# Kernel optimization log

Hardware: AMD Instinct MI355X
Metric: run time of the kernel (lower is better)

Reference implementation:

```python
import jax, jax.numpy as jnp
import numpy as np

TOP_K = 0.7  # fraction of highest-loss samples kept


def setup_inputs() -> dict:
    key = jax.random.key(0)
    k1, k2 = jax.random.split(key)
    N, C = 262144, 128
    inp = jax.random.normal(k1, (N, C), dtype=jnp.float32)
    tgt = jax.random.randint(k2, (N,), 0, C, dtype=jnp.int64)
    return {"input": inp, "target": tgt}


def reference(input, target):
    # log-softmax over classes, one stable pass
    logp = jax.nn.log_softmax(input, axis=-1)  # [N, C]
    # per-row NLL: -logp[i, target[i]]
    per_row = -jnp.take_along_axis(logp, target[:, None], axis=-1)[:, 0]  # [N]
    k = int(TOP_K * per_row.shape[0])
    top_vals, _ = jax.lax.top_k(per_row, k)  # k largest losses
    return jnp.mean(top_vals)
```

## Files before the change

### kernel.cpp

```cpp
#include <hip/hip_runtime.h>


#define NCLASS 128
#define NREP 8

struct Scalars {
  unsigned sel1, sel2;
  unsigned cnt_above;
  int krem;
  unsigned thr_bits;
  unsigned pad[11];
};

__device__ __forceinline__ unsigned suffix_incl_u(unsigned x, int lane) {
#pragma unroll
  for (int off = 1; off < 64; off <<= 1) {
    unsigned v = __shfl_down(x, off, 64);
    if (lane + off < 64) x += v;
  }
  return x;
}

__global__ __launch_bounds__(256) void loss_hist_kernel(
    const float* __restrict__ x, const int* __restrict__ tgt,
    float* __restrict__ losses, unsigned* __restrict__ hist1, int N) {
  __shared__ unsigned lh[4096];
  for (int i = threadIdx.x; i < 4096; i += 256) lh[i] = 0;
  __syncthreads();

  const int lane = threadIdx.x & 63;
  const int j = lane & 7;
  const int r = lane >> 3;
  const int gw = blockIdx.x * 4 + (threadIdx.x >> 6);
  const int W = gridDim.x * 4;

  for (int base = gw; base * 8 < N; base += W) {
    const int row = base * 8 + r;
    const float4* rp = (const float4*)(x + (size_t)row * NCLASS);
    float4 a = rp[j];
    float4 b = rp[j + 8];
    float4 c = rp[j + 16];
    float4 d = rp[j + 24];
    int t = tgt[row];
    float xt = x[(size_t)row * NCLASS + t];

    float m = fmaxf(fmaxf(fmaxf(a.x, a.y), fmaxf(a.z, a.w)),
                    fmaxf(fmaxf(b.x, b.y), fmaxf(b.z, b.w)));
    m = fmaxf(m, fmaxf(fmaxf(c.x, c.y), fmaxf(c.z, c.w)));
    m = fmaxf(m, fmaxf(fmaxf(d.x, d.y), fmaxf(d.z, d.w)));
    m = fmaxf(m, __shfl_xor(m, 1, 64));
    m = fmaxf(m, __shfl_xor(m, 2, 64));
    m = fmaxf(m, __shfl_xor(m, 4, 64));

    float s = __expf(a.x - m) + __expf(a.y - m) + __expf(a.z - m) + __expf(a.w - m)
            + __expf(b.x - m) + __expf(b.y - m) + __expf(b.z - m) + __expf(b.w - m)
            + __expf(c.x - m) + __expf(c.y - m) + __expf(c.z - m) + __expf(c.w - m)
            + __expf(d.x - m) + __expf(d.y - m) + __expf(d.z - m) + __expf(d.w - m);
    s += __shfl_xor(s, 1, 64);
    s += __shfl_xor(s, 2, 64);
    s += __shfl_xor(s, 4, 64);

    if (j == 0) {
      float loss = fmaxf(__logf(s) + m - xt, 0.0f);
      losses[row] = loss;
      atomicAdd(&lh[__float_as_uint(loss) >> 20], 1u);
    }
  }
  __syncthreads();
  unsigned* h = hist1 + (size_t)(blockIdx.x & (NREP - 1)) * 4096;
  for (int i = threadIdx.x; i < 4096; i += 256) {
    unsigned v = lh[i];
    if (v) atomicAdd(&h[i], v);
  }
}

__global__ __launch_bounds__(256) void hist_refine_kernel(
    const float* __restrict__ losses, const Scalars* __restrict__ sc,
    unsigned* __restrict__ hist, int N, int phase) {
  __shared__ unsigned lh[1024];
  for (int i = threadIdx.x; i < 1024; i += 256) lh[i] = 0;
  __syncthreads();
  unsigned prefix, shift;
  if (phase == 1) { prefix = sc->sel1; shift = 20; }
  else { prefix = (sc->sel1 << 10) | sc->sel2; shift = 10; }
  const unsigned sub_shift = shift - 10;
  const float4* L4 = (const float4*)losses;
  const int n4 = N >> 2;
  for (int idx = blockIdx.x * 256 + threadIdx.x; idx < n4; idx += gridDim.x * 256) {
    float4 v = L4[idx];
    unsigned b;
    b = __float_as_uint(v.x); if ((b >> shift) == prefix) atomicAdd(&lh[(b >> sub_shift) & 1023u], 1u);
    b = __float_as_uint(v.y); if ((b >> shift) == prefix) atomicAdd(&lh[(b >> sub_shift) & 1023u], 1u);
    b = __float_as_uint(v.z); if ((b >> shift) == prefix) atomicAdd(&lh[(b >> sub_shift) & 1023u], 1u);
    b = __float_as_uint(v.w); if ((b >> shift) == prefix) atomicAdd(&lh[(b >> sub_shift) & 1023u], 1u);
  }
  __syncthreads();
  unsigned* h = hist + (size_t)(blockIdx.x & (NREP - 1)) * 1024;
  for (int i = threadIdx.x; i < 1024; i += 256) {
    unsigned v = lh[i];
    if (v) atomicAdd(&h[i], v);
  }
}

__global__ void scan_kernel(const unsigned* __restrict__ hist, Scalars* sc,
                            int nbins, int phase, int K) {
  const int lane = threadIdx.x;
  const int bpt = nbins >> 6;
  const int Ktar = (phase == 0) ? K : sc->krem;

  unsigned csum = 0;
  for (int rr = 0; rr < NREP; ++rr) {
    const uint4* h4 = (const uint4*)(hist + (size_t)rr * nbins + lane * bpt);
    for (int i = 0; i < (bpt >> 2); ++i) {
      uint4 q = h4[i];
      csum += q.x + q.y + q.z + q.w;
    }
  }
  unsigned suf = suffix_incl_u(csum, lane);
  unsigned long long mask = __ballot(suf >= (unsigned)Ktar);
  int c = 63 - __builtin_clzll(mask);
  unsigned above_excl = suf - csum;
  unsigned aboveC = __shfl(above_excl, c, 64);

  unsigned h = 0;
  if (lane < bpt)
    for (int rr = 0; rr < NREP; ++rr) h += hist[(size_t)rr * nbins + c * bpt + lane];
  unsigned suf2 = suffix_incl_u(h, lane);
  unsigned long long mask2 = __ballot((lane < bpt) && (aboveC + suf2 >= (unsigned)Ktar));
  int u = 63 - __builtin_clzll(mask2);
  unsigned hU = __shfl(h, u, 64);
  unsigned suf2U = __shfl(suf2, u, 64);
  unsigned above = aboveC + suf2U - hU;
  int bin = c * bpt + u;

  if (lane == 0) {
    if (phase == 0) {
      sc->sel1 = (unsigned)bin; sc->cnt_above = above; sc->krem = Ktar - (int)above;
    } else if (phase == 1) {
      sc->sel2 = (unsigned)bin; sc->cnt_above += above; sc->krem = Ktar - (int)above;
    } else {
      sc->thr_bits = (sc->sel1 << 20) | (sc->sel2 << 10) | (unsigned)bin;
      sc->cnt_above += above;
    }
  }
}

__global__ __launch_bounds__(256) void sum_topk_kernel(
    const float* __restrict__ losses, const Scalars* __restrict__ sc,
    double* __restrict__ partials, int N) {
  const unsigned thr = sc->thr_bits;
  double acc = 0.0;
  const float4* L4 = (const float4*)losses;
  const int n4 = N >> 2;
  for (int idx = blockIdx.x * 256 + threadIdx.x; idx < n4; idx += gridDim.x * 256) {
    float4 v = L4[idx];
    if (__float_as_uint(v.x) > thr) acc += v.x;
    if (__float_as_uint(v.y) > thr) acc += v.y;
    if (__float_as_uint(v.z) > thr) acc += v.z;
    if (__float_as_uint(v.w) > thr) acc += v.w;
  }
#pragma unroll
  for (int off = 32; off > 0; off >>= 1) acc += __shfl_down(acc, off, 64);
  __shared__ double wsum[4];
  if ((threadIdx.x & 63) == 0) wsum[threadIdx.x >> 6] = acc;
  __syncthreads();
  if (threadIdx.x == 0)
    partials[blockIdx.x] = wsum[0] + wsum[1] + wsum[2] + wsum[3];
}

__global__ void finalize_kernel(const double* __restrict__ partials,
                                const Scalars* __restrict__ sc,
                                float* __restrict__ out, int K, int npart) {
  const int lane = threadIdx.x;
  double s = 0.0;
  for (int i = lane; i < npart; i += 64) s += partials[i];
#pragma unroll
  for (int off = 32; off > 0; off >>= 1) s += __shfl_down(s, off, 64);
  if (lane == 0) {
    double thr = (double)__uint_as_float(sc->thr_bits);
    double mean = (s + (double)(K - (int)sc->cnt_above) * thr) / (double)K;
    *out = (float)mean;
  }
}

extern "C" void kernel_launch(void* const* d_in, const int* in_sizes, int n_in,
                              void* d_out, int out_size, void* d_ws, size_t ws_size,
                              hipStream_t stream) {
  const float* x = (const float*)d_in[0];
  const int* tgt = (const int*)d_in[1];
  float* out = (float*)d_out;
  const int N = in_sizes[1];
  const int K = (int)(0.7 * (double)N);

  char* ws = (char*)d_ws;
  const size_t OFF_H1 = (size_t)N * 4;
  const size_t OFF_H2 = OFF_H1 + (size_t)NREP * 4096 * 4;
  const size_t OFF_H3 = OFF_H2 + (size_t)NREP * 1024 * 4;
  const size_t OFF_SC = OFF_H3 + (size_t)NREP * 1024 * 4;
  const size_t OFF_PT = OFF_SC + 256;

  float* losses = (float*)ws;
  unsigned* hist1 = (unsigned*)(ws + OFF_H1);
  unsigned* hist2 = (unsigned*)(ws + OFF_H2);
  unsigned* hist3 = (unsigned*)(ws + OFF_H3);
  Scalars* sc = (Scalars*)(ws + OFF_SC);
  double* partials = (double*)(ws + OFF_PT);

  hipMemsetAsync(ws + OFF_H1, 0, OFF_PT - OFF_H1, stream);

  loss_hist_kernel<<<512, 256, 0, stream>>>(x, tgt, losses, hist1, N);
  scan_kernel<<<1, 64, 0, stream>>>(hist1, sc, 4096, 0, K);
  hist_refine_kernel<<<64, 256, 0, stream>>>(losses, sc, hist2, N, 1);
  scan_kernel<<<1, 64, 0, stream>>>(hist2, sc, 1024, 1, K);
  hist_refine_kernel<<<64, 256, 0, stream>>>(losses, sc, hist3, N, 2);
  scan_kernel<<<1, 64, 0, stream>>>(hist3, sc, 1024, 2, K);
  sum_topk_kernel<<<128, 256, 0, stream>>>(losses, sc, partials, N);
  finalize_kernel<<<1, 64, 0, stream>>>(partials, sc, out, K, 128);
}
```

Measured before the change: 228.2 us.

## Fuse all phases into one cooperative persistent kernel with grid syncs

Replaces the memset plus eight separate kernel launches with one cooperative mega-kernel that runs loss computation, three radix-histogram refinement passes, scans, the top-k sum and finalisation, separated by grid-wide syncs. The grid is sized from occupancy queries so every CU is filled, and histogram zeroing moves inside the kernel. This removes per-launch overhead and the small single-block scan launches between phases. In exchange it adds eight grid barriers and host-side attribute and occupancy queries on every call, and falls back to the old launch path if cooperative launch is unavailable.

```diff
diff --git a/kernel.cpp b/kernel.cpp
--- a/kernel.cpp
+++ b/kernel.cpp
@@ -1,15 +1,19 @@
 #include <hip/hip_runtime.h>
+#include <hip/hip_cooperative_groups.h>
+
+namespace cg = cooperative_groups;
 
 
 #define NCLASS 128
 #define NREP 8
+#define TPB 256
+#define MAXGRID 2048
 
 struct Scalars {
   unsigned sel1, sel2;
   unsigned cnt_above;
   int krem;
   unsigned thr_bits;
-  unsigned pad[11];
 };
 
 __device__ __forceinline__ unsigned suffix_incl_u(unsigned x, int lane) {
@@ -21,89 +25,8 @@
   return x;
 }
 
-__global__ __launch_bounds__(256) void loss_hist_kernel(
-    const float* __restrict__ x, const int* __restrict__ tgt,
-    float* __restrict__ losses, unsigned* __restrict__ hist1, int N) {
-  __shared__ unsigned lh[4096];
-  for (int i = threadIdx.x; i < 4096; i += 256) lh[i] = 0;
-  __syncthreads();
-
-  const int lane = threadIdx.x & 63;
-  const int j = lane & 7;
-  const int r = lane >> 3;
-  const int gw = blockIdx.x * 4 + (threadIdx.x >> 6);
-  const int W = gridDim.x * 4;
-
-  for (int base = gw; base * 8 < N; base += W) {
-    const int row = base * 8 + r;
-    const float4* rp = (const float4*)(x + (size_t)row * NCLASS);
-    float4 a = rp[j];
-    float4 b = rp[j + 8];
-    float4 c = rp[j + 16];
-    float4 d = rp[j + 24];
-    int t = tgt[row];
-    float xt = x[(size_t)row * NCLASS + t];
-
-    float m = fmaxf(fmaxf(fmaxf(a.x, a.y), fmaxf(a.z, a.w)),
-                    fmaxf(fmaxf(b.x, b.y), fmaxf(b.z, b.w)));
-    m = fmaxf(m, fmaxf(fmaxf(c.x, c.y), fmaxf(c.z, c.w)));
-    m = fmaxf(m, fmaxf(fmaxf(d.x, d.y), fmaxf(d.z, d.w)));
-    m = fmaxf(m, __shfl_xor(m, 1, 64));
-    m = fmaxf(m, __shfl_xor(m, 2, 64));
-    m = fmaxf(m, __shfl_xor(m, 4, 64));
-
-    float s = __expf(a.x - m) + __expf(a.y - m) + __expf(a.z - m) + __expf(a.w - m)
-            + __expf(b.x - m) + __expf(b.y - m) + __expf(b.z - m) + __expf(b.w - m)
-            + __expf(c.x - m) + __expf(c.y - m) + __expf(c.z - m) + __expf(c.w - m)
-            + __expf(d.x - m) + __expf(d.y - m) + __expf(d.z - m) + __expf(d.w - m);
-    s += __shfl_xor(s, 1, 64);
-    s += __shfl_xor(s, 2, 64);
-    s += __shfl_xor(s, 4, 64);
-
-    if (j == 0) {
-      float loss = fmaxf(__logf(s) + m - xt, 0.0f);
-      losses[row] = loss;
-      atomicAdd(&lh[__float_as_uint(loss) >> 20], 1u);
-    }
-  }
-  __syncthreads();
-  unsigned* h = hist1 + (size_t)(blockIdx.x & (NREP - 1)) * 4096;
-  for (int i = threadIdx.x; i < 4096; i += 256) {
-    unsigned v = lh[i];
-    if (v) atomicAdd(&h[i], v);
-  }
-}
-
-__global__ __launch_bounds__(256) void hist_refine_kernel(
-    const float* __restrict__ losses, const Scalars* __restrict__ sc,
-    unsigned* __restrict__ hist, int N, int phase) {
-  __shared__ unsigned lh[1024];
-  for (int i = threadIdx.x; i < 1024; i += 256) lh[i] = 0;
-  __syncthreads();
-  unsigned prefix, shift;
-  if (phase == 1) { prefix = sc->sel1; shift = 20; }
-  else { prefix = (sc->sel1 << 10) | sc->sel2; shift = 10; }
-  const unsigned sub_shift = shift - 10;
-  const float4* L4 = (const float4*)losses;
-  const int n4 = N >> 2;
-  for (int idx = blockIdx.x * 256 + threadIdx.x; idx < n4; idx += gridDim.x * 256) {
-    float4 v = L4[idx];
-    unsigned b;
-    b = __float_as_uint(v.x); if ((b >> shift) == prefix) atomicAdd(&lh[(b >> sub_shift) & 1023u], 1u);
-    b = __float_as_uint(v.y); if ((b >> shift) == prefix) atomicAdd(&lh[(b >> sub_shift) & 1023u], 1u);
-    b = __float_as_uint(v.z); if ((b >> shift) == prefix) atomicAdd(&lh[(b >> sub_shift) & 1023u], 1u);
-    b = __float_as_uint(v.w); if ((b >> shift) == prefix) atomicAdd(&lh[(b >> sub_shift) & 1023u], 1u);
-  }
-  __syncthreads();
-  unsigned* h = hist + (size_t)(blockIdx.x & (NREP - 1)) * 1024;
-  for (int i = threadIdx.x; i < 1024; i += 256) {
-    unsigned v = lh[i];
-    if (v) atomicAdd(&h[i], v);
-  }
-}
-
-__global__ void scan_kernel(const unsigned* __restrict__ hist, Scalars* sc,
-                            int nbins, int phase, int K) {
+__device__ void scan_phase(const unsigned* __restrict__ hist, Scalars* sc,
+                           int nbins, int phase, int K) {
   const int lane = threadIdx.x;
   const int bpt = nbins >> 6;
   const int Ktar = (phase == 0) ? K : sc->krem;
@@ -145,14 +68,235 @@
   }
 }
 
-__global__ __launch_bounds__(256) void sum_topk_kernel(
+__device__ __forceinline__ void loss_hist_body(
+    const float* __restrict__ x, const int* __restrict__ tgt,
+    float* __restrict__ losses, unsigned* __restrict__ hist1,
+    unsigned* lh, int N, int nblocks) {
+  const int lane = threadIdx.x & 63;
+  const int j = lane & 7;
+  const int r = lane >> 3;
+  const int gw = blockIdx.x * (TPB / 64) + (threadIdx.x >> 6);
+  const int W = nblocks * (TPB / 64);
+  for (int base = gw; base * 8 < N; base += W) {
+    const int row = base * 8 + r;
+    const float4* rp = (const float4*)(x + (size_t)row * NCLASS);
+    float4 a = rp[j];
+    float4 b = rp[j + 8];
+    float4 c = rp[j + 16];
+    float4 d = rp[j + 24];
+    int t = tgt[row];
+    float xt = x[(size_t)row * NCLASS + t];
+
+    float m = fmaxf(fmaxf(fmaxf(a.x, a.y), fmaxf(a.z, a.w)),
+                    fmaxf(fmaxf(b.x, b.y), fmaxf(b.z, b.w)));
+    m = fmaxf(m, fmaxf(fmaxf(c.x, c.y), fmaxf(c.z, c.w)));
+    m = fmaxf(m, fmaxf(fmaxf(d.x, d.y), fmaxf(d.z, d.w)));
+    m = fmaxf(m, __shfl_xor(m, 1, 64));
+    m = fmaxf(m, __shfl_xor(m, 2, 64));
+    m = fmaxf(m, __shfl_xor(m, 4, 64));
+
+    float s = __expf(a.x - m) + __expf(a.y - m) + __expf(a.z - m) + __expf(a.w - m)
+            + __expf(b.x - m) + __expf(b.y - m) + __expf(b.z - m) + __expf(b.w - m)
+            + __expf(c.x - m) + __expf(c.y - m) + __expf(c.z - m) + __expf(c.w - m)
+            + __expf(d.x - m) + __expf(d.y - m) + __expf(d.z - m) + __expf(d.w - m);
+    s += __shfl_xor(s, 1, 64);
+    s += __shfl_xor(s, 2, 64);
+    s += __shfl_xor(s, 4, 64);
+
+    if (j == 0) {
+      float loss = fmaxf(__logf(s) + m - xt, 0.0f);
+      losses[row] = loss;
+      atomicAdd(&lh[__float_as_uint(loss) >> 20], 1u);
+    }
+  }
+  __syncthreads();
+  unsigned* h = hist1 + (size_t)(blockIdx.x & (NREP - 1)) * 4096;
+  for (int i = threadIdx.x; i < 4096; i += TPB) {
+    unsigned v = lh[i];
+    if (v) atomicAdd(&h[i], v);
+  }
+}
+
+__global__ __launch_bounds__(TPB, 2) void mega_kernel(
+    const float* __restrict__ x, const int* __restrict__ tgt,
+    float* __restrict__ losses, unsigned* __restrict__ hist1,
+    unsigned* __restrict__ hist2, unsigned* __restrict__ hist3,
+    Scalars* __restrict__ sc, double* __restrict__ partials,
+    float* __restrict__ out, int N, int K) {
+  cg::grid_group grid = cg::this_grid();
+  __shared__ unsigned lh[4096];
+  __shared__ double dsm[TPB / 64];
+
+  const int lane = threadIdx.x & 63;
+  const int G = gridDim.x;
+
+  for (int i = threadIdx.x; i < 4096; i += TPB) lh[i] = 0;
+  for (int i = blockIdx.x * TPB + threadIdx.x; i < NREP * 4096; i += G * TPB)
+    hist1[i] = 0;
+  __syncthreads();
+  grid.sync();
+
+  loss_hist_body(x, tgt, losses, hist1, lh, N, G);
+  __threadfence();
+  grid.sync();
+
+  if (blockIdx.x == 0) {
+    if (threadIdx.x < 64) scan_phase(hist1, sc, 4096, 0, K);
+  } else {
+    for (int i = (blockIdx.x - 1) * TPB + threadIdx.x; i < NREP * 1024;
+         i += (G - 1) * TPB)
+      hist2[i] = 0;
+  }
+  __threadfence();
+  grid.sync();
+
+  const float4* L4 = (const float4*)losses;
+  const int n4 = N >> 2;
+
+  {
+    for (int i = threadIdx.x; i < 1024; i += TPB) lh[i] = 0;
+    __syncthreads();
+    const unsigned prefix = sc->sel1;
+    for (int idx = blockIdx.x * TPB + threadIdx.x; idx < n4; idx += G * TPB) {
+      float4 v = L4[idx];
+      unsigned b;
+      b = __float_as_uint(v.x); if ((b >> 20) == prefix) atomicAdd(&lh[(b >> 10) & 1023u], 1u);
+      b = __float_as_uint(v.y); if ((b >> 20) == prefix) atomicAdd(&lh[(b >> 10) & 1023u], 1u);
+      b = __float_as_uint(v.z); if ((b >> 20) == prefix) atomicAdd(&lh[(b >> 10) & 1023u], 1u);
+      b = __float_as_uint(v.w); if ((b >> 20) == prefix) atomicAdd(&lh[(b >> 10) & 1023u], 1u);
+    }
+    __syncthreads();
+    unsigned* h = hist2 + (size_t)(blockIdx.x & (NREP - 1)) * 1024;
+    for (int i = threadIdx.x; i < 1024; i += TPB) {
+      unsigned v = lh[i];
+      if (v) atomicAdd(&h[i], v);
+    }
+  }
+  __threadfence();
+  grid.sync();
+
+  if (blockIdx.x == 0) {
+    if (threadIdx.x < 64) scan_phase(hist2, sc, 1024, 1, K);
+  } else {
+    for (int i = (blockIdx.x - 1) * TPB + threadIdx.x; i < NREP * 1024;
+         i += (G - 1) * TPB)
+      hist3[i] = 0;
+  }
+  __threadfence();
+  grid.sync();
+
+  {
+    for (int i = threadIdx.x; i < 1024; i += TPB) lh[i] = 0;
+    __syncthreads();
+    const unsigned prefix = (sc->sel1 << 10) | sc->sel2;
+    for (int idx = blockIdx.x * TPB + threadIdx.x; idx < n4; idx += G * TPB) {
+      float4 v = L4[idx];
+      unsigned b;
+      b = __float_as_uint(v.x); if ((b >> 10) == prefix) atomicAdd(&lh[b & 1023u], 1u);
+      b = __float_as_uint(v.y); if ((b >> 10) == prefix) atomicAdd(&lh[b & 1023u], 1u);
+      b = __float_as_uint(v.z); if ((b >> 10) == prefix) atomicAdd(&lh[b & 1023u], 1u);
+      b = __float_as_uint(v.w); if ((b >> 10) == prefix) atomicAdd(&lh[b & 1023u], 1u);
+    }
+    __syncthreads();
+    unsigned* h = hist3 + (size_t)(blockIdx.x & (NREP - 1)) * 1024;
+    for (int i = threadIdx.x; i < 1024; i += TPB) {
+      unsigned v = lh[i];
+      if (v) atomicAdd(&h[i], v);
+    }
+  }
+  __threadfence();
+  grid.sync();
+
+  if (blockIdx.x == 0 && threadIdx.x < 64) scan_phase(hist3, sc, 1024, 2, K);
+  __threadfence();
+  grid.sync();
+
+  {
+    const unsigned thr = sc->thr_bits;
+    double acc = 0.0;
+    for (int idx = blockIdx.x * TPB + threadIdx.x; idx < n4; idx += G * TPB) {
+      float4 v = L4[idx];
+      if (__float_as_uint(v.x) > thr) acc += v.x;
+      if (__float_as_uint(v.y) > thr) acc += v.y;
+      if (__float_as_uint(v.z) > thr) acc += v.z;
+      if (__float_as_uint(v.w) > thr) acc += v.w;
+    }
+#pragma unroll
+    for (int off = 32; off > 0; off >>= 1) acc += __shfl_down(acc, off, 64);
+    if (lane == 0) dsm[threadIdx.x >> 6] = acc;
+    __syncthreads();
+    if (threadIdx.x == 0)
+      partials[blockIdx.x] = dsm[0] + dsm[1] + dsm[2] + dsm[3];
+  }
+  __threadfence();
+  grid.sync();
+
+  if (blockIdx.x == 0) {
+    double s = 0.0;
+    for (int i = threadIdx.x; i < G; i += TPB) s += partials[i];
+#pragma unroll
+    for (int off = 32; off > 0; off >>= 1) s += __shfl_down(s, off, 64);
+    if (lane == 0) dsm[threadIdx.x >> 6] = s;
+    __syncthreads();
+    if (threadIdx.x == 0) {
+      double thrv = (double)__uint_as_float(sc->thr_bits);
+      double mean = (dsm[0] + dsm[1] + dsm[2] + dsm[3] +
+                     (double)(K - (int)sc->cnt_above) * thrv) / (double)K;
+      *out = (float)mean;
+    }
+  }
+}
+
+__global__ __launch_bounds__(TPB) void loss_hist_kernel(
+    const float* __restrict__ x, const int* __restrict__ tgt,
+    float* __restrict__ losses, unsigned* __restrict__ hist1, int N, int nblocks) {
+  __shared__ unsigned lh[4096];
+  for (int i = threadIdx.x; i < 4096; i += TPB) lh[i] = 0;
+  __syncthreads();
+  loss_hist_body(x, tgt, losses, hist1, lh, N, nblocks);
+}
+
+__global__ void scan_kernel(const unsigned* __restrict__ hist, Scalars* sc,
+                            int nbins, int phase, int K) {
+  scan_phase(hist, sc, nbins, phase, K);
+}
+
+__global__ __launch_bounds__(TPB) void hist_refine_kernel(
+    const float* __restrict__ losses, const Scalars* __restrict__ sc,
+    unsigned* __restrict__ hist, int N, int phase) {
+  __shared__ unsigned lh[1024];
+  for (int i = threadIdx.x; i < 1024; i += TPB) lh[i] = 0;
+  __syncthreads();
+  unsigned prefix, shift;
+  if (phase == 1) { prefix = sc->sel1; shift = 20; }
+  else { prefix = (sc->sel1 << 10) | sc->sel2; shift = 10; }
+  const unsigned sub_shift = shift - 10;
+  const float4* L4 = (const float4*)losses;
+  const int n4 = N >> 2;
+  for (int idx = blockIdx.x * TPB + threadIdx.x; idx < n4; idx += gridDim.x * TPB) {
+    float4 v = L4[idx];
+    unsigned b;
+    b = __float_as_uint(v.x); if ((b >> shift) == prefix) atomicAdd(&lh[(b >> sub_shift) & 1023u], 1u);
+    b = __float_as_uint(v.y); if ((b >> shift) == prefix) atomicAdd(&lh[(b >> sub_shift) & 1023u], 1u);
+    b = __float_as_uint(v.z); if ((b >> shift) == prefix) atomicAdd(&lh[(b >> sub_shift) & 1023u], 1u);
+    b = __float_as_uint(v.w); if ((b >> shift) == prefix) atomicAdd(&lh[(b >> sub_shift) & 1023u], 1u);
+  }
+  __syncthreads();
+  unsigned* h = hist + (size_t)(blockIdx.x & (NREP - 1)) * 1024;
+  for (int i = threadIdx.x; i < 1024; i += TPB) {
+    unsigned v = lh[i];
+    if (v) atomicAdd(&h[i], v);
+  }
+}
+
+__global__ __launch_bounds__(TPB) void sum_topk_kernel(
     const float* __restrict__ losses, const Scalars* __restrict__ sc,
     double* __restrict__ partials, int N) {
   const unsigned thr = sc->thr_bits;
   double acc = 0.0;
   const float4* L4 = (const float4*)losses;
   const int n4 = N >> 2;
-  for (int idx = blockIdx.x * 256 + threadIdx.x; idx < n4; idx += gridDim.x * 256) {
+  for (int idx = blockIdx.x * TPB + threadIdx.x; idx < n4; idx += gridDim.x * TPB) {
     float4 v = L4[idx];
     if (__float_as_uint(v.x) > thr) acc += v.x;
     if (__float_as_uint(v.y) > thr) acc += v.y;
@@ -189,8 +333,8 @@
   const float* x = (const float*)d_in[0];
   const int* tgt = (const int*)d_in[1];
   float* out = (float*)d_out;
-  const int N = in_sizes[1];
-  const int K = (int)(0.7 * (double)N);
+  int N = in_sizes[1];
+  int K = (int)(0.7 * (double)N);
 
   char* ws = (char*)d_ws;
   const size_t OFF_H1 = (size_t)N * 4;
@@ -206,14 +350,35 @@
   Scalars* sc = (Scalars*)(ws + OFF_SC);
   double* partials = (double*)(ws + OFF_PT);
 
+  int dev = 0;
+  (void)hipGetDevice(&dev);
+  int coop = 0;
+  (void)hipDeviceGetAttribute(&coop, hipDeviceAttributeCooperativeLaunch, dev);
+  int nCU = 0;
+  (void)hipDeviceGetAttribute(&nCU, hipDeviceAttributeMultiprocessorCount, dev);
+  int blocksPerCU = 0;
+  (void)hipOccupancyMaxActiveBlocksPerMultiprocessor(&blocksPerCU,
+                                                     (const void*)mega_kernel,
+                                                     TPB, 0);
+  int grid = nCU * blocksPerCU;
+  if (grid > MAXGRID) grid = MAXGRID;
+
+  if (coop && grid >= 64) {
+    void* args[] = {&x, &tgt, &losses, &hist1, &hist2, &hist3, &sc, &partials,
+                    &out, &N, &K};
+    hipError_t err = hipLaunchCooperativeKernel((const void*)mega_kernel,
+                                                dim3(grid), dim3(TPB), args, 0,
+                                                stream);
+    if (err == hipSuccess) return;
+  }
+
   hipMemsetAsync(ws + OFF_H1, 0, OFF_PT - OFF_H1, stream);
-
-  loss_hist_kernel<<<512, 256, 0, stream>>>(x, tgt, losses, hist1, N);
+  loss_hist_kernel<<<512, TPB, 0, stream>>>(x, tgt, losses, hist1, N, 512);
   scan_kernel<<<1, 64, 0, stream>>>(hist1, sc, 4096, 0, K);
-  hist_refine_kernel<<<64, 256, 0, stream>>>(losses, sc, hist2, N, 1);
+  hist_refine_kernel<<<64, TPB, 0, stream>>>(losses, sc, hist2, N, 1);
   scan_kernel<<<1, 64, 0, stream>>>(hist2, sc, 1024, 1, K);
-  hist_refine_kernel<<<64, 256, 0, stream>>>(losses, sc, hist3, N, 2);
+  hist_refine_kernel<<<64, TPB, 0, stream>>>(losses, sc, hist3, N, 2);
   scan_kernel<<<1, 64, 0, stream>>>(hist3, sc, 1024, 2, K);
-  sum_topk_kernel<<<128, 256, 0, stream>>>(losses, sc, partials, N);
+  sum_topk_kernel<<<128, TPB, 0, stream>>>(losses, sc, partials, N);
   finalize_kernel<<<1, 64, 0, stream>>>(partials, sc, out, K, 128);
 }
```

Result: slower. 886.6 us (+288.6%).

## Fuse scans into producer kernels via last-block tickets and merge refine passes

Applied to the files above, without the earlier changes.

Removes the separate single-wave scan and finalize kernels: the last block to finish each histogram/sum kernel (detected with an atomic ticket) performs the scan or final reduction. The two refine passes are merged into one by also building a 1M-entry global fine histogram of the low 20 bits, so the third-level bin is found without another pass over losses. This cuts the launch count from eight to three plus one memset. The cost is a larger memset (4 MB), global atomics on the fine histogram for rows in the selected bucket, and the refine stage now runs at grid 128 instead of 64.

```diff
diff --git a/kernel.cpp b/kernel.cpp
--- a/kernel.cpp
+++ b/kernel.cpp
@@ -3,14 +3,23 @@
 
 #define NCLASS 128
 #define NREP 8
+#define TPB 256
+#define LOSS_GRID 512
+#define SMALL_GRID 128
 
 struct Scalars {
   unsigned sel1, sel2;
   unsigned cnt_above;
   int krem;
   unsigned thr_bits;
-  unsigned pad[11];
 };
+
+__device__ __forceinline__ unsigned aload_u(const unsigned* p) {
+  return __hip_atomic_load(p, __ATOMIC_RELAXED, __HIP_MEMORY_SCOPE_AGENT);
+}
+__device__ __forceinline__ double aload_d(const double* p) {
+  return __hip_atomic_load(p, __ATOMIC_RELAXED, __HIP_MEMORY_SCOPE_AGENT);
+}
 
 __device__ __forceinline__ unsigned suffix_incl_u(unsigned x, int lane) {
 #pragma unroll
@@ -21,19 +30,58 @@
   return x;
 }
 
-__global__ __launch_bounds__(256) void loss_hist_kernel(
+__device__ __forceinline__ bool block_is_last(unsigned* ticket, unsigned nblocks) {
+  __shared__ int amLast;
+  __threadfence();
+  __syncthreads();
+  if (threadIdx.x == 0)
+    amLast = (__hip_atomic_fetch_add(ticket, 1u, __ATOMIC_ACQ_REL,
+                                     __HIP_MEMORY_SCOPE_AGENT) == nblocks - 1)
+                 ? 1 : 0;
+  __syncthreads();
+  return amLast != 0;
+}
+
+__device__ __forceinline__ void scan_desc(const unsigned* hist, int nbins,
+                                          int nrep, unsigned Ktar,
+                                          int* bin_out, unsigned* above_out) {
+  const int lane = threadIdx.x;
+  const int bpt = nbins >> 6;
+  unsigned csum = 0;
+  for (int rr = 0; rr < nrep; ++rr) {
+    const unsigned* hp = hist + (size_t)rr * nbins + lane * bpt;
+    for (int i = 0; i < bpt; ++i) csum += aload_u(hp + i);
+  }
+  unsigned suf = suffix_incl_u(csum, lane);
+  unsigned long long mask = __ballot(suf >= Ktar);
+  int c = 63 - __builtin_clzll(mask);
+  unsigned aboveC = __shfl(suf - csum, c, 64);
+
+  unsigned h = 0;
+  if (lane < bpt)
+    for (int rr = 0; rr < nrep; ++rr)
+      h += aload_u(hist + (size_t)rr * nbins + c * bpt + lane);
+  unsigned suf2 = suffix_incl_u(h, lane);
+  unsigned long long mask2 = __ballot((lane < bpt) && (aboveC + suf2 >= Ktar));
+  int u = 63 - __builtin_clzll(mask2);
+  unsigned above = aboveC + __shfl(suf2 - h, u, 64);
+  *bin_out = c * bpt + u;
+  *above_out = above;
+}
+
+__global__ __launch_bounds__(TPB) void loss_hist_kernel(
     const float* __restrict__ x, const int* __restrict__ tgt,
-    float* __restrict__ losses, unsigned* __restrict__ hist1, int N) {
+    float* __restrict__ losses, unsigned* __restrict__ hist1,
+    Scalars* __restrict__ sc, unsigned* __restrict__ tickets, int N, int K) {
   __shared__ unsigned lh[4096];
-  for (int i = threadIdx.x; i < 4096; i += 256) lh[i] = 0;
+  for (int i = threadIdx.x; i < 4096; i += TPB) lh[i] = 0;
   __syncthreads();
 
   const int lane = threadIdx.x & 63;
   const int j = lane & 7;
   const int r = lane >> 3;
-  const int gw = blockIdx.x * 4 + (threadIdx.x >> 6);
-  const int W = gridDim.x * 4;
-
+  const int gw = blockIdx.x * (TPB / 64) + (threadIdx.x >> 6);
+  const int W = LOSS_GRID * (TPB / 64);
   for (int base = gw; base * 8 < N; base += W) {
     const int row = base * 8 + r;
     const float4* rp = (const float4*)(x + (size_t)row * NCLASS);
@@ -68,91 +116,78 @@
   }
   __syncthreads();
   unsigned* h = hist1 + (size_t)(blockIdx.x & (NREP - 1)) * 4096;
-  for (int i = threadIdx.x; i < 4096; i += 256) {
+  for (int i = threadIdx.x; i < 4096; i += TPB) {
     unsigned v = lh[i];
     if (v) atomicAdd(&h[i], v);
   }
-}
-
-__global__ __launch_bounds__(256) void hist_refine_kernel(
-    const float* __restrict__ losses, const Scalars* __restrict__ sc,
-    unsigned* __restrict__ hist, int N, int phase) {
+
+  if (block_is_last(&tickets[0], LOSS_GRID) && threadIdx.x < 64) {
+    int bin; unsigned above;
+    scan_desc(hist1, 4096, NREP, (unsigned)K, &bin, &above);
+    if (threadIdx.x == 0) {
+      sc->sel1 = (unsigned)bin;
+      sc->cnt_above = above;
+      sc->krem = K - (int)above;
+    }
+  }
+}
+
+__global__ __launch_bounds__(TPB) void refine_kernel(
+    const float* __restrict__ losses, unsigned* __restrict__ hist2,
+    unsigned* __restrict__ fine, Scalars* __restrict__ sc,
+    unsigned* __restrict__ tickets, int N) {
   __shared__ unsigned lh[1024];
-  for (int i = threadIdx.x; i < 1024; i += 256) lh[i] = 0;
-  __syncthreads();
-  unsigned prefix, shift;
-  if (phase == 1) { prefix = sc->sel1; shift = 20; }
-  else { prefix = (sc->sel1 << 10) | sc->sel2; shift = 10; }
-  const unsigned sub_shift = shift - 10;
+  for (int i = threadIdx.x; i < 1024; i += TPB) lh[i] = 0;
+  __syncthreads();
+
+  const unsigned prefix = sc->sel1;
   const float4* L4 = (const float4*)losses;
   const int n4 = N >> 2;
-  for (int idx = blockIdx.x * 256 + threadIdx.x; idx < n4; idx += gridDim.x * 256) {
+  for (int idx = blockIdx.x * TPB + threadIdx.x; idx < n4;
+       idx += SMALL_GRID * TPB) {
     float4 v = L4[idx];
     unsigned b;
-    b = __float_as_uint(v.x); if ((b >> shift) == prefix) atomicAdd(&lh[(b >> sub_shift) & 1023u], 1u);
-    b = __float_as_uint(v.y); if ((b >> shift) == prefix) atomicAdd(&lh[(b >> sub_shift) & 1023u], 1u);
-    b = __float_as_uint(v.z); if ((b >> shift) == prefix) atomicAdd(&lh[(b >> sub_shift) & 1023u], 1u);
-    b = __float_as_uint(v.w); if ((b >> shift) == prefix) atomicAdd(&lh[(b >> sub_shift) & 1023u], 1u);
-  }
-  __syncthreads();
-  unsigned* h = hist + (size_t)(blockIdx.x & (NREP - 1)) * 1024;
-  for (int i = threadIdx.x; i < 1024; i += 256) {
+    b = __float_as_uint(v.x);
+    if ((b >> 20) == prefix) { atomicAdd(&lh[(b >> 10) & 1023u], 1u); atomicAdd(&fine[b & 0xFFFFFu], 1u); }
+    b = __float_as_uint(v.y);
+    if ((b >> 20) == prefix) { atomicAdd(&lh[(b >> 10) & 1023u], 1u); atomicAdd(&fine[b & 0xFFFFFu], 1u); }
+    b = __float_as_uint(v.z);
+    if ((b >> 20) == prefix) { atomicAdd(&lh[(b >> 10) & 1023u], 1u); atomicAdd(&fine[b & 0xFFFFFu], 1u); }
+    b = __float_as_uint(v.w);
+    if ((b >> 20) == prefix) { atomicAdd(&lh[(b >> 10) & 1023u], 1u); atomicAdd(&fine[b & 0xFFFFFu], 1u); }
+  }
+  __syncthreads();
+  unsigned* h = hist2 + (size_t)(blockIdx.x & (NREP - 1)) * 1024;
+  for (int i = threadIdx.x; i < 1024; i += TPB) {
     unsigned v = lh[i];
     if (v) atomicAdd(&h[i], v);
   }
-}
-
-__global__ void scan_kernel(const unsigned* __restrict__ hist, Scalars* sc,
-                            int nbins, int phase, int K) {
-  const int lane = threadIdx.x;
-  const int bpt = nbins >> 6;
-  const int Ktar = (phase == 0) ? K : sc->krem;
-
-  unsigned csum = 0;
-  for (int rr = 0; rr < NREP; ++rr) {
-    const uint4* h4 = (const uint4*)(hist + (size_t)rr * nbins + lane * bpt);
-    for (int i = 0; i < (bpt >> 2); ++i) {
-      uint4 q = h4[i];
-      csum += q.x + q.y + q.z + q.w;
-    }
-  }
-  unsigned suf = suffix_incl_u(csum, lane);
-  unsigned long long mask = __ballot(suf >= (unsigned)Ktar);
-  int c = 63 - __builtin_clzll(mask);
-  unsigned above_excl = suf - csum;
-  unsigned aboveC = __shfl(above_excl, c, 64);
-
-  unsigned h = 0;
-  if (lane < bpt)
-    for (int rr = 0; rr < NREP; ++rr) h += hist[(size_t)rr * nbins + c * bpt + lane];
-  unsigned suf2 = suffix_incl_u(h, lane);
-  unsigned long long mask2 = __ballot((lane < bpt) && (aboveC + suf2 >= (unsigned)Ktar));
-  int u = 63 - __builtin_clzll(mask2);
-  unsigned hU = __shfl(h, u, 64);
-  unsigned suf2U = __shfl(suf2, u, 64);
-  unsigned above = aboveC + suf2U - hU;
-  int bin = c * bpt + u;
-
-  if (lane == 0) {
-    if (phase == 0) {
-      sc->sel1 = (unsigned)bin; sc->cnt_above = above; sc->krem = Ktar - (int)above;
-    } else if (phase == 1) {
-      sc->sel2 = (unsigned)bin; sc->cnt_above += above; sc->krem = Ktar - (int)above;
-    } else {
-      sc->thr_bits = (sc->sel1 << 20) | (sc->sel2 << 10) | (unsigned)bin;
-      sc->cnt_above += above;
-    }
-  }
-}
-
-__global__ __launch_bounds__(256) void sum_topk_kernel(
+
+  if (block_is_last(&tickets[1], SMALL_GRID) && threadIdx.x < 64) {
+    int bin; unsigned above;
+    scan_desc(hist2, 1024, NREP, (unsigned)sc->krem, &bin, &above);
+    unsigned sel2 = (unsigned)bin;
+    unsigned krem2 = (unsigned)sc->krem - above;
+    unsigned cnt2 = sc->cnt_above + above;
+    int bin3; unsigned above3;
+    scan_desc(fine + (size_t)sel2 * 1024, 1024, 1, krem2, &bin3, &above3);
+    if (threadIdx.x == 0) {
+      sc->thr_bits = (sc->sel1 << 20) | (sel2 << 10) | (unsigned)bin3;
+      sc->cnt_above = cnt2 + above3;
+    }
+  }
+}
+
+__global__ __launch_bounds__(TPB) void sum_topk_kernel(
     const float* __restrict__ losses, const Scalars* __restrict__ sc,
-    double* __restrict__ partials, int N) {
+    double* __restrict__ partials, unsigned* __restrict__ tickets,
+    float* __restrict__ out, int N, int K) {
   const unsigned thr = sc->thr_bits;
   double acc = 0.0;
   const float4* L4 = (const float4*)losses;
   const int n4 = N >> 2;
-  for (int idx = blockIdx.x * 256 + threadIdx.x; idx < n4; idx += gridDim.x * 256) {
+  for (int idx = blockIdx.x * TPB + threadIdx.x; idx < n4;
+       idx += SMALL_GRID * TPB) {
     float4 v = L4[idx];
     if (__float_as_uint(v.x) > thr) acc += v.x;
     if (__float_as_uint(v.y) > thr) acc += v.y;
@@ -161,25 +196,25 @@
   }
 #pragma unroll
   for (int off = 32; off > 0; off >>= 1) acc += __shfl_down(acc, off, 64);
-  __shared__ double wsum[4];
-  if ((threadIdx.x & 63) == 0) wsum[threadIdx.x >> 6] = acc;
+  __shared__ double dsm[TPB / 64];
+  if ((threadIdx.x & 63) == 0) dsm[threadIdx.x >> 6] = acc;
   __syncthreads();
   if (threadIdx.x == 0)
-    partials[blockIdx.x] = wsum[0] + wsum[1] + wsum[2] + wsum[3];
-}
-
-__global__ void finalize_kernel(const double* __restrict__ partials,
-                                const Scalars* __restrict__ sc,
-                                float* __restrict__ out, int K, int npart) {
-  const int lane = threadIdx.x;
-  double s = 0.0;
-  for (int i = lane; i < npart; i += 64) s += partials[i];
+    partials[blockIdx.x] = dsm[0] + dsm[1] + dsm[2] + dsm[3];
+
+  if (block_is_last(&tickets[2], SMALL_GRID)) {
+    double s = 0.0;
+    for (int i = threadIdx.x; i < SMALL_GRID; i += TPB) s += aload_d(&partials[i]);
 #pragma unroll
-  for (int off = 32; off > 0; off >>= 1) s += __shfl_down(s, off, 64);
-  if (lane == 0) {
-    double thr = (double)__uint_as_float(sc->thr_bits);
-    double mean = (s + (double)(K - (int)sc->cnt_above) * thr) / (double)K;
-    *out = (float)mean;
+    for (int off = 32; off > 0; off >>= 1) s += __shfl_down(s, off, 64);
+    if ((threadIdx.x & 63) == 0) dsm[threadIdx.x >> 6] = s;
+    __syncthreads();
+    if (threadIdx.x == 0) {
+      double thrv = (double)__uint_as_float(sc->thr_bits);
+      double mean = (dsm[0] + dsm[1] + dsm[2] + dsm[3] +
+                     (double)(K - (int)sc->cnt_above) * thrv) / (double)K;
+      *out = (float)mean;
+    }
   }
 }
 
@@ -189,31 +224,31 @@
   const float* x = (const float*)d_in[0];
   const int* tgt = (const int*)d_in[1];
   float* out = (float*)d_out;
-  const int N = in_sizes[1];
-  const int K = (int)(0.7 * (double)N);
+  int N = in_sizes[1];
+  int K = (int)(0.7 * (double)N);
 
   char* ws = (char*)d_ws;
   const size_t OFF_H1 = (size_t)N * 4;
   const size_t OFF_H2 = OFF_H1 + (size_t)NREP * 4096 * 4;
-  const size_t OFF_H3 = OFF_H2 + (size_t)NREP * 1024 * 4;
-  const size_t OFF_SC = OFF_H3 + (size_t)NREP * 1024 * 4;
-  const size_t OFF_PT = OFF_SC + 256;
+  const size_t OFF_FN = OFF_H2 + (size_t)NREP * 1024 * 4;
+  const size_t OFF_SC = OFF_FN + (size_t)(1u << 20) * 4;
+  const size_t OFF_TK = OFF_SC + 64;
+  const size_t OFF_PT = OFF_TK + 64;
 
   float* losses = (float*)ws;
   unsigned* hist1 = (unsigned*)(ws + OFF_H1);
   unsigned* hist2 = (unsigned*)(ws + OFF_H2);
-  unsigned* hist3 = (unsigned*)(ws + OFF_H3);
+  unsigned* fine = (unsigned*)(ws + OFF_FN);
   Scalars* sc = (Scalars*)(ws + OFF_SC);
+  unsigned* tickets = (unsigned*)(ws + OFF_TK);
   double* partials = (double*)(ws + OFF_PT);
 
   hipMemsetAsync(ws + OFF_H1, 0, OFF_PT - OFF_H1, stream);
 
-  loss_hist_kernel<<<512, 256, 0, stream>>>(x, tgt, losses, hist1, N);
-  scan_kernel<<<1, 64, 0, stream>>>(hist1, sc, 4096, 0, K);
-  hist_refine_kernel<<<64, 256, 0, stream>>>(losses, sc, hist2, N, 1);
-  scan_kernel<<<1, 64, 0, stream>>>(hist2, sc, 1024, 1, K);
-  hist_refine_kernel<<<64, 256, 0, stream>>>(losses, sc, hist3, N, 2);
-  scan_kernel<<<1, 64, 0, stream>>>(hist3, sc, 1024, 2, K);
-  sum_topk_kernel<<<128, 256, 0, stream>>>(losses, sc, partials, N);
-  finalize_kernel<<<1, 64, 0, stream>>>(partials, sc, out, K, 128);
-}
+  loss_hist_kernel<<<LOSS_GRID, TPB, 0, stream>>>(x, tgt, losses, hist1, sc,
+                                                  tickets, N, K);
+  refine_kernel<<<SMALL_GRID, TPB, 0, stream>>>(losses, hist2, fine, sc,
+                                                tickets, N);
+  sum_topk_kernel<<<SMALL_GRID, TPB, 0, stream>>>(losses, sc, partials,
+                                                  tickets, out, N, K);
+}
```

New measurement: 308.4 us. 1.35x slower.
